# Optimization experiments

Measured on AMD Instinct MI355X. Metric: run time of the kernel, lower is better.

The kernel has to match this reference:

```python
import jax, jax.numpy as jnp
import numpy as np

D_MODEL = 1024
NUM_HEADS = 16
D_HEAD = D_MODEL // NUM_HEADS


def setup_inputs() -> dict:
    key = jax.random.key(0)
    ks = jax.random.split(key, 5)
    b, n = 4, 2048
    x = jax.random.normal(ks[0], (b, n, D_MODEL), dtype=jnp.float32)
    s = 1.0 / np.sqrt(D_MODEL)
    w_qkv = jax.random.normal(ks[1], (D_MODEL, 3 * D_MODEL), dtype=jnp.float32) * s
    b_qkv = jax.random.normal(ks[2], (3 * D_MODEL,), dtype=jnp.float32) * 0.01
    w_out = jax.random.normal(ks[3], (D_MODEL, D_MODEL), dtype=jnp.float32) * s
    b_out = jax.random.normal(ks[4], (D_MODEL,), dtype=jnp.float32) * 0.01
    return {"x": x, "w_qkv": w_qkv, "b_qkv": b_qkv, "w_out": w_out, "b_out": b_out}


def reference(x, w_qkv, b_qkv, w_out, b_out):
    b, n, _ = x.shape
    h, d = NUM_HEADS, D_HEAD
    scale = d ** -0.5
    qkv = x @ w_qkv + b_qkv                       # [b, n, 3*d_model]
    # split as (qkv, h, d) on the feature axis, matching 'b n (qkv h d)'
    qkv = qkv.reshape(b, n, 3, h, d).transpose(2, 0, 3, 1, 4)  # [3, b, h, n, d]
    q, k, v = qkv[0], qkv[1], qkv[2]
    dots = jnp.einsum('bhid,bhjd->bhij', q, k) * scale
    causal = jnp.tril(jnp.ones((n, n), dtype=bool))
    dots = jnp.where(causal[None, None], dots, -jnp.inf)
    attn = jax.nn.softmax(dots, axis=-1)
    out = jnp.einsum('bhij,bhjd->bhid', attn, v)
    out = out.transpose(0, 2, 1, 3).reshape(b, n, h * d)
    return out @ w_out + b_out
```

## Files before the change

kernel.cpp:

```cpp
#include <hip/hip_runtime.h>
#include <hip/hip_bf16.h>
#include <stdint.h>

typedef unsigned short u16;
typedef __attribute__((ext_vector_type(8))) short bf16x8;
typedef __attribute__((ext_vector_type(4))) float f32x4;
typedef __attribute__((ext_vector_type(16))) float f32x16;
typedef __attribute__((ext_vector_type(4))) short s16x4;
typedef __attribute__((ext_vector_type(2))) unsigned u32x2;

#define SEQ   2048
#define BATCH 4

#define MFMA16(a,b,c) __builtin_amdgcn_mfma_f32_16x16x32_bf16(a,b,c,0,0,0)
#define MFMA32(a,b,c) __builtin_amdgcn_mfma_f32_32x32x16_bf16(a,b,c,0,0,0)
#define EXP2F __builtin_amdgcn_exp2f

__device__ __forceinline__ u16 f2bf(float f) {
  union { float f; uint32_t u; } c{f};
  uint32_t r = c.u + 0x7fffu + ((c.u >> 16) & 1u);
  return (u16)(r >> 16);
}

__device__ __forceinline__ void gll16(const void* g, void* l) {
  __builtin_amdgcn_global_load_lds((const __attribute__((address_space(1))) void*)g,
                                   (__attribute__((address_space(3))) void*)l,
                                   16, 0, 0);
}

__device__ __forceinline__ void plswap(uint32_t &a, uint32_t &b) {
  u32x2 r = __builtin_amdgcn_permlane32_swap(a, b, false, false);
  a = r[0]; b = r[1];
}
__device__ __forceinline__ float xhalf_max(float v) {
  union { float f; uint32_t u; } c{v};
  u32x2 r = __builtin_amdgcn_permlane32_swap(c.u, c.u, false, false);
  union { uint32_t u; float f; } x{r[0]}, y{r[1]};
  return fmaxf(x.f, y.f);
}

__global__ __launch_bounds__(256) void k_prep(const float* __restrict__ x,
                                              u16* __restrict__ xbf,
                                              const float* __restrict__ wqkv,
                                              u16* __restrict__ wqkvT,
                                              const float* __restrict__ wout,
                                              u16* __restrict__ woutT) {
  __shared__ float tl[32][33];
  const int bid = blockIdx.x, t = threadIdx.x;
  if (bid < 4096) {
    int i = (bid * 256 + t) * 8;
    float4 a = *(const float4*)(x + i);
    float4 b = *(const float4*)(x + i + 4);
    union { u16 u[8]; bf16x8 v; } r;
    r.u[0] = f2bf(a.x); r.u[1] = f2bf(a.y); r.u[2] = f2bf(a.z); r.u[3] = f2bf(a.w);
    r.u[4] = f2bf(b.x); r.u[5] = f2bf(b.y); r.u[6] = f2bf(b.z); r.u[7] = f2bf(b.w);
    *(bf16x8*)(xbf + i) = r.v;
    return;
  }
  const float* in; u16* out; int N, idx, nx;
  if (bid < 4096 + 3072) { in = wqkv; out = wqkvT; N = 3072; idx = bid - 4096; nx = 96; }
  else                   { in = wout; out = woutT; N = 1024; idx = bid - 7168; nx = 32; }
  const int K = 1024;
  const int c0 = (idx % nx) * 32, r0 = (idx / nx) * 32;
  const int tx = t & 31, ty = t >> 5;
#pragma unroll
  for (int j = 0; j < 32; j += 8)
    tl[ty + j][tx] = in[(size_t)(r0 + ty + j) * N + c0 + tx];
  __syncthreads();
#pragma unroll
  for (int j = 0; j < 32; j += 8)
    out[(size_t)(c0 + ty + j) * K + r0 + tx] = f2bf(tl[tx][ty + j]);
}

#define SBAR  asm volatile("s_barrier" ::: "memory")
#define LGKM0 asm volatile("s_waitcnt lgkmcnt(0)" ::: "memory")
#define VM2   asm volatile("s_waitcnt vmcnt(2)" ::: "memory")
#define VM0   asm volatile("s_waitcnt vmcnt(0)" ::: "memory")
#define FEN   asm volatile("" ::: "memory")

template<int OUT_F32>
__global__ __launch_bounds__(512, 2) void k_gemm256(const u16* __restrict__ A,
                                                    const u16* __restrict__ BT,
                                                    const float* __restrict__ bias,
                                                    void* __restrict__ Cv,
                                                    int N, int K, int NT, int TN) {
  __shared__ alignas(16) char LDS[98304];
  const int t = threadIdx.x;
  const int l = t & 63, w = t >> 6;
  const int wm = w >> 2, wn = w & 3;
  const int lr = l & 15, lg = l >> 4;

  const int nwg = gridDim.x;
  const int cpx = nwg >> 3;
  const int sb = (blockIdx.x & 7) * cpx + (blockIdx.x >> 3);
  const int brow = (sb / TN) * 256, bcol = (sb % TN) * 128;

  auto stageA = [&](int c, int h, int tt) {
#pragma unroll
    for (int i = 0; i < 2; i++) {
      int s = t + i * 512;
      int r = s >> 3, cg = s & 7;
      int grow = brow + (r >> 6) * 128 + h * 64 + (r & 63);
      int gk = tt * 64 + ((cg ^ (r & 7)) * 8);
      gll16(A + (size_t)grow * K + gk, LDS + c * 49152 + h * 16384 + s * 16);
    }
  };
  auto stageB = [&](int c, int tt) {
#pragma unroll
    for (int i = 0; i < 2; i++) {
      int s = t + i * 512;
      int r = s >> 3, cg = s & 7;
      int grow = bcol + r;
      int gk = tt * 64 + ((cg ^ (r & 7)) * 8);
      gll16(BT + (size_t)grow * K + gk, LDS + c * 49152 + 32768 + s * 16);
    }
  };

  f32x4 acc[8][2] = {};
  bf16x8 afr[4], bfr[2];

#define READ_A(c, h, ks)                                                       \
  {                                                                            \
    const char* baseA = LDS + (c) * 49152 + (h) * 16384 + (wm * 64) * 128;     \
    _Pragma("unroll") for (int mi = 0; mi < 4; mi++)                           \
      afr[mi] = *(const bf16x8*)(baseA + (mi * 16 + lr) * 128 +                \
                                 ((((ks) * 4 + lg) ^ (lr & 7)) * 16));         \
  }
#define READ_B(c, ks)                                                          \
  {                                                                            \
    const char* baseB = LDS + (c) * 49152 + 32768 + (wn * 32) * 128;           \
    _Pragma("unroll") for (int ni = 0; ni < 2; ni++)                           \
      bfr[ni] = *(const bf16x8*)(baseB + (ni * 16 + lr) * 128 +                \
                                 ((((ks) * 4 + lg) ^ (lr & 7)) * 16));         \
  }
#define DO_MFMA(H)                                                             \
  {                                                                            \
    __builtin_amdgcn_s_setprio(1);                                             \
    _Pragma("unroll") for (int mi = 0; mi < 4; mi++)                           \
      _Pragma("unroll") for (int ni = 0; ni < 2; ni++)                         \
        acc[(H)*4 + mi][ni] = MFMA16(afr[mi], bfr[ni], acc[(H)*4 + mi][ni]);   \
    __builtin_amdgcn_s_setprio(0);                                             \
  }

  stageA(0, 0, 0); FEN;
  stageB(0, 0);    FEN;
  stageA(0, 1, 0); FEN;
  VM2; SBAR;

  for (int tt = 0; tt < NT; tt++) {
    const int c = tt & 1;
    if (tt + 1 < NT) { stageA(c ^ 1, 0, tt + 1); FEN; }
    READ_A(c, 0, 0); READ_B(c, 0);
    DO_MFMA(0);
    if (tt + 1 < NT) { VM2; } else { VM0; }
    LGKM0; SBAR;
    if (tt + 1 < NT) { stageB(c ^ 1, tt + 1); FEN; }
    READ_A(c, 1, 0);
    DO_MFMA(1);
    if (tt + 1 < NT) { stageA(c ^ 1, 1, tt + 1); FEN; }
    READ_A(c, 1, 1); READ_B(c, 1);
    DO_MFMA(1);
    READ_A(c, 0, 1);
    DO_MFMA(0);
    VM2;
    LGKM0; SBAR;
  }

  const int r0 = brow + wm * 128 + lg * 4;
  const int c0 = bcol + wn * 32 + lr;
#pragma unroll
  for (int ni = 0; ni < 2; ni++) {
    float bv = bias[c0 + ni * 16];
#pragma unroll
    for (int mig = 0; mig < 8; mig++) {
      const int row = r0 + mig * 16;
#pragma unroll
      for (int r = 0; r < 4; r++) {
        float v = acc[mig][ni][r] + bv;
        size_t off = (size_t)(row + r) * N + c0 + ni * 16;
        if (OUT_F32) ((float*)Cv)[off] = v;
        else         ((u16*)Cv)[off]   = f2bf(v);
      }
    }
  }
}
#undef READ_A
#undef READ_B
#undef DO_MFMA

__global__ __launch_bounds__(256) void k_trV(const u16* __restrict__ qkv,
                                             u16* __restrict__ vT) {
  __shared__ u16 s[32][33];
  int tx = threadIdx.x & 31, ty = threadIdx.x >> 5;
  int n0 = blockIdx.x * 32, d0 = blockIdx.y * 32, bh = blockIdx.z;
  int b = bh >> 4, h = bh & 15;
#pragma unroll
  for (int j = 0; j < 32; j += 8)
    s[ty + j][tx] = qkv[(size_t)(b * SEQ + n0 + ty + j) * 3072 + 2048 + h * 64 + d0 + tx];
  __syncthreads();
#pragma unroll
  for (int j = 0; j < 32; j += 8)
    vT[(size_t)(bh * 64 + d0 + ty + j) * SEQ + n0 + tx] = s[tx][ty + j];
}

__global__ __launch_bounds__(256) void k_attn(const u16* __restrict__ qkv,
                                              const u16* __restrict__ vT,
                                              u16* __restrict__ outp) {
  __shared__ alignas(16) char SB[2][16384];
  const int t = threadIdx.x, l = t & 63, w = t >> 6;
  const int hi = l >> 5, q = l & 31;
  const int h = blockIdx.x, qp = blockIdx.y, b = blockIdx.z;
  const int bh = b * 16 + h;
  const int srow = t >> 3;
  const int csw = ((t & 7) * 16) ^ ((srow & 7) << 4);
  const int swz = (q & 7) << 4;
  const float SC = 0.18033688011112042f;
  union { u16 u[8]; bf16x8 v; } onesu;
#pragma unroll
  for (int i = 0; i < 8; i++) onesu.u[i] = 0x3F80;
  const bf16x8 ones = onesu.v;

  auto STAGE = [&](char* buf, int kv0) {
    char* lK = buf + w * 1024;
    char* lV = buf + 8192 + w * 1024;
    gll16(qkv + (size_t)(b * SEQ + kv0 + srow) * 3072 + 1024 + h * 64 + (csw >> 1), lK);
    gll16(qkv + (size_t)(b * SEQ + kv0 + srow + 32) * 3072 + 1024 + h * 64 + (csw >> 1), lK + 4096);
    gll16(vT + (size_t)(bh * 64 + srow) * SEQ + kv0 + (csw >> 1), lV);
    gll16(vT + (size_t)(bh * 64 + srow + 32) * SEQ + kv0 + (csw >> 1), lV + 4096);
  };

  for (int tsel = 0; tsel < 2; tsel++) {
    const int qt = tsel ? (15 - qp) : qp;
    const int qr0 = qt * 128 + w * 32;
    const int qg = qr0 + q;
    bf16x8 qf[4];
#pragma unroll
    for (int c = 0; c < 4; c++)
      qf[c] = *(const bf16x8*)(qkv + (size_t)(b * SEQ + qg) * 3072 + h * 64 + c * 16 + hi * 8);
    f32x16 o0 = {}, o1 = {}, lvac = {};
    float m_run = -1e30f;
    const int nkv = 2 * qt + 2;

    STAGE(SB[0], 0);
    for (int j = 0; j < nkv; j++) {
      const int kv0 = j * 64;
      __syncthreads();
      if (j + 1 < nkv) STAGE(SB[(j + 1) & 1], kv0 + 64);
      const char* Kb = SB[j & 1];
      const char* Vb = Kb + 8192;

      if (kv0 <= qr0 + 31) {
        f32x16 st0 = {}, st1 = {};
        __builtin_amdgcn_s_setprio(1);
#pragma unroll
        for (int c = 0; c < 4; c++) {
          const int cb = c * 32 + hi * 16;
          bf16x8 k0 = *(const bf16x8*)(Kb + q * 128 + (cb ^ swz));
          bf16x8 k1 = *(const bf16x8*)(Kb + (32 + q) * 128 + (cb ^ swz));
          st0 = MFMA32(k0, qf[c], st0);
          st1 = MFMA32(k1, qf[c], st1);
        }
        __builtin_amdgcn_s_setprio(0);
        if (kv0 + 63 > qr0) {
#pragma unroll
          for (int r = 0; r < 16; r++) {
            const int krow = (r & 3) + 8 * (r >> 2) + 4 * hi;
            if (kv0 + krow > qg)      st0[r] = -1e30f;
            if (kv0 + 32 + krow > qg) st1[r] = -1e30f;
          }
        }
        float tmx[16];
#pragma unroll
        for (int r = 0; r < 16; r++) tmx[r] = fmaxf(st0[r], st1[r]);
        float v0 = fmaxf(fmaxf(tmx[0], tmx[1]), tmx[2]);
        float v1 = fmaxf(fmaxf(tmx[3], tmx[4]), tmx[5]);
        float v2 = fmaxf(fmaxf(tmx[6], tmx[7]), tmx[8]);
        float v3 = fmaxf(fmaxf(tmx[9], tmx[10]), tmx[11]);
        float v4 = fmaxf(fmaxf(tmx[12], tmx[13]), tmx[14]);
        float v5 = fmaxf(fmaxf(v0, v1), tmx[15]);
        float v6 = fmaxf(fmaxf(v2, v3), v4);
        float v7 = fmaxf(v5, v6);
        const float vs = xhalf_max(v7) * SC;
        if (__any(vs > m_run + 8.0f)) {
          float mnew = fmaxf(m_run, vs);
          float corr = EXP2F(m_run - mnew);
          m_run = mnew;
#pragma unroll
          for (int r = 0; r < 16; r++) { o0[r] *= corr; o1[r] *= corr; lvac[r] *= corr; }
        }
        f32x16 e0 = st0 * SC - m_run;
        f32x16 e1 = st1 * SC - m_run;
        f32x16 p0, p1;
#pragma unroll
        for (int r = 0; r < 16; r++) { p0[r] = EXP2F(e0[r]); p1[r] = EXP2F(e1[r]); }
#pragma unroll
        for (int khb = 0; khb < 2; khb++) {
          uint32_t pk[8];
#pragma unroll
          for (int ii = 0; ii < 8; ii++) {
            float lo = khb ? p1[2 * ii] : p0[2 * ii];
            float hf = khb ? p1[2 * ii + 1] : p0[2 * ii + 1];
            asm("v_cvt_pk_bf16_f32 %0, %1, %2" : "=v"(pk[ii]) : "v"(lo), "v"(hf));
          }
          plswap(pk[0], pk[2]); plswap(pk[1], pk[3]);
          plswap(pk[4], pk[6]); plswap(pk[5], pk[7]);
          union { uint32_t u[4]; bf16x8 v; } be, bo;
          be.u[0] = pk[0]; be.u[1] = pk[1]; be.u[2] = pk[2]; be.u[3] = pk[3];
          bo.u[0] = pk[4]; bo.u[1] = pk[5]; bo.u[2] = pk[6]; bo.u[3] = pk[7];
          __builtin_amdgcn_s_setprio(1);
#pragma unroll
          for (int kti = 0; kti < 2; kti++) {
            const int cb = (khb * 2 + kti) * 32 + hi * 16;
            bf16x8 vv0 = *(const bf16x8*)(Vb + q * 128 + (cb ^ swz));
            bf16x8 vv1 = *(const bf16x8*)(Vb + (32 + q) * 128 + (cb ^ swz));
            bf16x8 pb = kti ? bo.v : be.v;
            o0 = MFMA32(vv0, pb, o0);
            o1 = MFMA32(vv1, pb, o1);
            lvac = MFMA32(ones, pb, lvac);
          }
          __builtin_amdgcn_s_setprio(0);
        }
      }
    }
    __syncthreads();
    const float invl = 1.0f / lvac[0];
#pragma unroll
    for (int dh = 0; dh < 2; dh++)
#pragma unroll
      for (int jq = 0; jq < 4; jq++) {
        union { u16 u[4]; s16x4 v; } pk4;
#pragma unroll
        for (int r = 0; r < 4; r++)
          pk4.u[r] = f2bf((dh ? o1[4 * jq + r] : o0[4 * jq + r]) * invl);
        *(s16x4*)(outp + (size_t)(b * SEQ + qg) * 1024 + h * 64 + dh * 32 + jq * 8 + hi * 4) = pk4.v;
      }
  }
}

extern "C" void kernel_launch(void* const* d_in, const int* in_sizes, int n_in,
                              void* d_out, int out_size, void* d_ws, size_t ws_size,
                              hipStream_t stream) {
  const float* x     = (const float*)d_in[0];
  const float* w_qkv = (const float*)d_in[1];
  const float* b_qkv = (const float*)d_in[2];
  const float* w_out = (const float*)d_in[3];
  const float* b_out = (const float*)d_in[4];

  char* ws = (char*)d_ws;
  u16* xbf   = (u16*)(ws);
  u16* wqkvT = (u16*)(ws + (16u << 20));
  u16* woutT = (u16*)(ws + (22u << 20));
  u16* qkvb  = (u16*)(ws + (24u << 20));
  u16* vTb   = (u16*)(ws + (72u << 20));

  k_prep<<<8192, 256, 0, stream>>>(x, xbf, w_qkv, wqkvT, w_out, woutT);
  k_gemm256<0><<<768, 512, 0, stream>>>(xbf, wqkvT, b_qkv, qkvb, 3072, 1024, 16, 24);
  k_trV <<<dim3(64, 2, 64), 256, 0, stream>>>(qkvb, vTb);
  k_attn<<<dim3(16, 8, 4), 256, 0, stream>>>(qkvb, vTb, xbf);
  k_gemm256<1><<<256, 512, 0, stream>>>(xbf, woutT, b_out, d_out, 1024, 1024, 16, 8);
}
```

Baseline: 174.9 us.

## Fuse V transpose into QKV GEMM epilogue and compute softmax denominator on VALU

```diff
diff --git a/kernel.cpp b/kernel.cpp
--- a/kernel.cpp
+++ b/kernel.cpp
@@ -37,6 +37,12 @@
   u32x2 r = __builtin_amdgcn_permlane32_swap(c.u, c.u, false, false);
   union { uint32_t u; float f; } x{r[0]}, y{r[1]};
   return fmaxf(x.f, y.f);
+}
+__device__ __forceinline__ float xhalf_add(float v) {
+  union { float f; uint32_t u; } c{v};
+  u32x2 r = __builtin_amdgcn_permlane32_swap(c.u, c.u, false, false);
+  union { uint32_t u; float f; } x{r[0]}, y{r[1]};
+  return x.f + y.f;
 }
 
 __global__ __launch_bounds__(256) void k_prep(const float* __restrict__ x,
@@ -78,11 +84,12 @@
 #define VM0   asm volatile("s_waitcnt vmcnt(0)" ::: "memory")
 #define FEN   asm volatile("" ::: "memory")
 
-template<int OUT_F32>
+template<int OUT_F32, int VSPLIT>
 __global__ __launch_bounds__(512, 2) void k_gemm256(const u16* __restrict__ A,
                                                     const u16* __restrict__ BT,
                                                     const float* __restrict__ bias,
                                                     void* __restrict__ Cv,
+                                                    u16* __restrict__ vT,
                                                     int N, int K, int NT, int TN) {
   __shared__ alignas(16) char LDS[98304];
   const int t = threadIdx.x;
@@ -170,16 +177,25 @@
   const int c0 = bcol + wn * 32 + lr;
 #pragma unroll
   for (int ni = 0; ni < 2; ni++) {
-    float bv = bias[c0 + ni * 16];
+    const int col = c0 + ni * 16;
+    float bv = bias[col];
 #pragma unroll
     for (int mig = 0; mig < 8; mig++) {
       const int row = r0 + mig * 16;
-#pragma unroll
-      for (int r = 0; r < 4; r++) {
-        float v = acc[mig][ni][r] + bv;
-        size_t off = (size_t)(row + r) * N + c0 + ni * 16;
-        if (OUT_F32) ((float*)Cv)[off] = v;
-        else         ((u16*)Cv)[off]   = f2bf(v);
+      if (VSPLIT && col >= 2048) {
+        const int bb = row >> 11, n0 = row & 2047;
+        union { u16 u[4]; s16x4 v; } pk4;
+#pragma unroll
+        for (int r = 0; r < 4; r++) pk4.u[r] = f2bf(acc[mig][ni][r] + bv);
+        *(s16x4*)(vT + ((size_t)(bb * 1024 + col - 2048) * SEQ + n0)) = pk4.v;
+      } else {
+#pragma unroll
+        for (int r = 0; r < 4; r++) {
+          float v = acc[mig][ni][r] + bv;
+          size_t off = (size_t)(row + r) * N + col;
+          if (OUT_F32) ((float*)Cv)[off] = v;
+          else         ((u16*)Cv)[off]   = f2bf(v);
+        }
       }
     }
   }
@@ -187,21 +203,6 @@
 #undef READ_A
 #undef READ_B
 #undef DO_MFMA
-
-__global__ __launch_bounds__(256) void k_trV(const u16* __restrict__ qkv,
-                                             u16* __restrict__ vT) {
-  __shared__ u16 s[32][33];
-  int tx = threadIdx.x & 31, ty = threadIdx.x >> 5;
-  int n0 = blockIdx.x * 32, d0 = blockIdx.y * 32, bh = blockIdx.z;
-  int b = bh >> 4, h = bh & 15;
-#pragma unroll
-  for (int j = 0; j < 32; j += 8)
-    s[ty + j][tx] = qkv[(size_t)(b * SEQ + n0 + ty + j) * 3072 + 2048 + h * 64 + d0 + tx];
-  __syncthreads();
-#pragma unroll
-  for (int j = 0; j < 32; j += 8)
-    vT[(size_t)(bh * 64 + d0 + ty + j) * SEQ + n0 + tx] = s[tx][ty + j];
-}
 
 __global__ __launch_bounds__(256) void k_attn(const u16* __restrict__ qkv,
                                               const u16* __restrict__ vT,
@@ -215,10 +216,6 @@
   const int csw = ((t & 7) * 16) ^ ((srow & 7) << 4);
   const int swz = (q & 7) << 4;
   const float SC = 0.18033688011112042f;
-  union { u16 u[8]; bf16x8 v; } onesu;
-#pragma unroll
-  for (int i = 0; i < 8; i++) onesu.u[i] = 0x3F80;
-  const bf16x8 ones = onesu.v;
 
   auto STAGE = [&](char* buf, int kv0) {
     char* lK = buf + w * 1024;
@@ -237,7 +234,7 @@
 #pragma unroll
     for (int c = 0; c < 4; c++)
       qf[c] = *(const bf16x8*)(qkv + (size_t)(b * SEQ + qg) * 3072 + h * 64 + c * 16 + hi * 8);
-    f32x16 o0 = {}, o1 = {}, lvac = {};
+    f32x16 o0 = {}, o1 = {}, lv = {};
     float m_run = -1e30f;
     const int nkv = 2 * qt + 2;
 
@@ -286,13 +283,14 @@
           float corr = EXP2F(m_run - mnew);
           m_run = mnew;
 #pragma unroll
-          for (int r = 0; r < 16; r++) { o0[r] *= corr; o1[r] *= corr; lvac[r] *= corr; }
+          for (int r = 0; r < 16; r++) { o0[r] *= corr; o1[r] *= corr; lv[r] *= corr; }
         }
         f32x16 e0 = st0 * SC - m_run;
         f32x16 e1 = st1 * SC - m_run;
         f32x16 p0, p1;
 #pragma unroll
         for (int r = 0; r < 16; r++) { p0[r] = EXP2F(e0[r]); p1[r] = EXP2F(e1[r]); }
+        lv += p0 + p1;
 #pragma unroll
         for (int khb = 0; khb < 2; khb++) {
           uint32_t pk[8];
@@ -316,14 +314,16 @@
             bf16x8 pb = kti ? bo.v : be.v;
             o0 = MFMA32(vv0, pb, o0);
             o1 = MFMA32(vv1, pb, o1);
-            lvac = MFMA32(ones, pb, lvac);
           }
           __builtin_amdgcn_s_setprio(0);
         }
       }
     }
     __syncthreads();
-    const float invl = 1.0f / lvac[0];
+    float ls = ((lv[0] + lv[1]) + (lv[2] + lv[3])) + ((lv[4] + lv[5]) + (lv[6] + lv[7]))
+             + ((lv[8] + lv[9]) + (lv[10] + lv[11])) + ((lv[12] + lv[13]) + (lv[14] + lv[15]));
+    ls = xhalf_add(ls);
+    const float invl = 1.0f / ls;
 #pragma unroll
     for (int dh = 0; dh < 2; dh++)
 #pragma unroll
@@ -354,8 +354,7 @@
   u16* vTb   = (u16*)(ws + (72u << 20));
 
   k_prep<<<8192, 256, 0, stream>>>(x, xbf, w_qkv, wqkvT, w_out, woutT);
-  k_gemm256<0><<<768, 512, 0, stream>>>(xbf, wqkvT, b_qkv, qkvb, 3072, 1024, 16, 24);
-  k_trV <<<dim3(64, 2, 64), 256, 0, stream>>>(qkvb, vTb);
+  k_gemm256<0, 1><<<768, 512, 0, stream>>>(xbf, wqkvT, b_qkv, qkvb, vTb, 3072, 1024, 16, 24);
   k_attn<<<dim3(16, 8, 4), 256, 0, stream>>>(qkvb, vTb, xbf);
-  k_gemm256<1><<<256, 512, 0, stream>>>(xbf, woutT, b_out, d_out, 1024, 1024, 16, 8);
-}
+  k_gemm256<1, 0><<<256, 512, 0, stream>>>(xbf, woutT, b_out, d_out, nullptr, 1024, 1024, 16, 8);
+}
```

After: 168.9 us. 3.4% less time.
